# Kernel tuning notes

Hardware: AMD Instinct MI355X
Metric: run time of the kernel (lower is better)

## Reference

```python
import jax, jax.numpy as jnp
import numpy as np

EPS = 1e-6
SEARCH_RANGE = 4  # K = 2*R+1 = 9


def setup_inputs() -> dict:
    key = jax.random.key(0)
    k1, k2, k3, k4 = jax.random.split(key, 4)
    B, C, H, W = 4, 128, 128, 240
    E = 64
    F_L = jax.random.normal(k1, (B, C, H, W), dtype=jnp.float32)
    F_R = jax.random.normal(k2, (B, C, H, W), dtype=jnp.float32)
    d0 = jax.random.uniform(k3, (B, 1, H, W), dtype=jnp.float32) * 64.0  # pixel disparity
    phi_w = jax.random.normal(k4, (E, C), dtype=jnp.float32) / np.sqrt(C)  # 1x1 conv weight
    return {"F_L": F_L, "F_R": F_R, "d0": d0, "phi_w": phi_w}


def _embed(x, phi_w):
    # 1x1 conv + channel L2 normalize (cosine embedding)
    y = jnp.einsum('ec,bchw->behw', phi_w, x)
    norm = jnp.sqrt(jnp.sum(y * y, axis=1, keepdims=True)) + EPS
    return y / norm


def reference(F_L, F_R, d0, phi_w):
    R = SEARCH_RANGE
    FL = _embed(F_L, phi_w)  # (B,E,H,W)
    FR = _embed(F_R, phi_w)
    B, E, H, W = FL.shape
    deltas = jnp.arange(-R, R + 1, dtype=FL.dtype)  # (K,)
    xx = jnp.arange(W, dtype=FL.dtype)  # base x grid
    # x' = x - (d0 + delta); align_corners=True grid round-trips to pixel coords exactly,
    # y coordinate is identity, so warp is 1D bilinear along W with border clamp.
    xprime = xx[None, None, None, :] - d0[:, None, 0, :, :] - deltas[None, :, None, None]  # (B,K,H,W)
    x0 = jnp.floor(xprime)
    w = xprime - x0  # bilinear weight
    i0 = jnp.clip(x0.astype(jnp.int32), 0, W - 1)
    i1 = jnp.clip(x0.astype(jnp.int32) + 1, 0, W - 1)
    FR_e = FR[:, None]  # (B,1,E,H,W)
    g0 = jnp.take_along_axis(FR_e, i0[:, :, None, :, :], axis=4)  # (B,K,E,H,W)
    g1 = jnp.take_along_axis(FR_e, i1[:, :, None, :, :], axis=4)
    FR_s = g0 * (1.0 - w)[:, :, None] + g1 * w[:, :, None]
    cost_vol = jnp.einsum('behw,bkehw->bkhw', FL, FR_s)  # (B,K,H,W)
    return cost_vol
```

## Files before the change

### kernel.cpp

```cpp
#include <hip/hip_runtime.h>

#define NB 4
#define NC 128
#define NH 128
#define NW 240
#define NE 64
#define NK 9
#define PLANE (NH*NW)
#define CHW (NC*PLANE)
#define XS 244

typedef __attribute__((ext_vector_type(8))) short short8;
typedef __attribute__((ext_vector_type(4))) float f32x4;

__device__ __forceinline__ unsigned short f2bf(float f){
  unsigned u = __float_as_uint(f);
  u += 0x7fffu + ((u>>16)&1u);
  return (unsigned short)(u>>16);
}
__device__ __forceinline__ float bfl(unsigned v){ return __uint_as_float(v<<16); }
__device__ __forceinline__ float bfh(unsigned v){ return __uint_as_float(v & 0xffff0000u); }

__global__ __launch_bounds__(256, 1)
void corr_kernel(const float* __restrict__ xL,
                 const float* __restrict__ xR,
                 const float* __restrict__ d0g,
                 const float* __restrict__ phig,
                 float* __restrict__ outg)
{
  __shared__ __attribute__((aligned(16))) unsigned short xs[NC*XS];
  __shared__ __attribute__((aligned(16))) unsigned short phis[NE*136];
  __shared__ __attribute__((aligned(16))) unsigned short FLb[NW*64];
  __shared__ __attribute__((aligned(16))) unsigned short FRb[NW*64];

  const int tid  = threadIdx.x;
  const int lane = tid & 63;
  const int wv   = tid >> 6;
  const int b    = blockIdx.x >> 7;
  const int h    = blockIdx.x & 127;
  const size_t base = (size_t)b*CHW + (size_t)h*NW;

  float d0v = 0.f;
  if (tid < NW) d0v = d0g[(b*NH + h)*NW + tid];

  #pragma unroll
  for (int i = 0; i < 8; ++i) {
    int idx = i*256 + tid;
    int e = idx >> 5, q = idx & 31;
    float4 v = *(const float4*)(phig + e*128 + 4*q);
    uint2 pk;
    pk.x = (unsigned)f2bf(v.x) | ((unsigned)f2bf(v.y) << 16);
    pk.y = (unsigned)f2bf(v.z) | ((unsigned)f2bf(v.w) << 16);
    *(uint2*)&phis[e*136 + 4*q] = pk;
  }

  #pragma unroll
  for (int i = 0; i < 30; ++i) {
    int idx = i*256 + tid;
    int c = idx / 60, s = idx - 60*c;
    float4 v = *(const float4*)(xL + base + (size_t)c*PLANE + 4*s);
    uint2 pk;
    pk.x = (unsigned)f2bf(v.x) | ((unsigned)f2bf(v.y) << 16);
    pk.y = (unsigned)f2bf(v.z) | ((unsigned)f2bf(v.w) << 16);
    *(uint2*)&xs[c*XS + 4*s] = pk;
  }
  __syncthreads();

  const int mrow = lane & 15;
  const int kg   = lane >> 4;
  const int nt0  = wv*4;

  auto gemm_norm = [&](unsigned short* dst) {
    f32x4 acc[4][4];
    #pragma unroll
    for (int i = 0; i < 4; ++i)
      #pragma unroll
      for (int mt = 0; mt < 4; ++mt)
        acc[i][mt] = (f32x4){0.f,0.f,0.f,0.f};

    #pragma unroll
    for (int ks = 0; ks < 4; ++ks) {
      short8 af[4];
      #pragma unroll
      for (int mt = 0; mt < 4; ++mt)
        af[mt] = *(const short8*)&phis[(16*mt + mrow)*136 + 32*ks + 8*kg];
      const int r0 = 32*ks + 8*kg;
      #pragma unroll
      for (int i = 0; i < 4; ++i) {
        int nt = nt0 + i;
        if (nt < 15) {
          int col = 16*nt + mrow;
          short8 bfv;
          #pragma unroll
          for (int j = 0; j < 8; ++j)
            bfv[j] = (short)xs[(r0 + j)*XS + col];
          #pragma unroll
          for (int mt = 0; mt < 4; ++mt)
            acc[i][mt] = __builtin_amdgcn_mfma_f32_16x16x32_bf16(af[mt], bfv, acc[i][mt], 0, 0, 0);
        }
      }
    }
    #pragma unroll
    for (int i = 0; i < 4; ++i) {
      int nt = nt0 + i;
      if (nt >= 15) continue;
      float ss = 0.f;
      #pragma unroll
      for (int mt = 0; mt < 4; ++mt)
        #pragma unroll
        for (int r = 0; r < 4; ++r)
          ss += acc[i][mt][r]*acc[i][mt][r];
      ss += __shfl_xor(ss, 16, 64);
      ss += __shfl_xor(ss, 32, 64);
      float inv = 1.f/(sqrtf(ss) + 1e-6f);
      int n = 16*nt + mrow;
      #pragma unroll
      for (int mt = 0; mt < 4; ++mt) {
        int e0 = 16*mt + 4*kg;
        ushort4 pk;
        pk.x = f2bf(acc[i][mt][0]*inv);
        pk.y = f2bf(acc[i][mt][1]*inv);
        pk.z = f2bf(acc[i][mt][2]*inv);
        pk.w = f2bf(acc[i][mt][3]*inv);
        int pos = n*64 + (((e0>>3) ^ (n&7))<<3) + (e0&7);
        *(ushort4*)&dst[pos] = pk;
      }
    }
  };

  gemm_norm(FLb);
  __syncthreads();

  #pragma unroll
  for (int i = 0; i < 30; ++i) {
    int idx = i*256 + tid;
    int c = idx / 60, s = idx - 60*c;
    float4 v = *(const float4*)(xR + base + (size_t)c*PLANE + 4*s);
    uint2 pk;
    pk.x = (unsigned)f2bf(v.x) | ((unsigned)f2bf(v.y) << 16);
    pk.y = (unsigned)f2bf(v.z) | ((unsigned)f2bf(v.w) << 16);
    *(uint2*)&xs[c*XS + 4*s] = pk;
  }
  __syncthreads();

  gemm_norm(FRb);
  __syncthreads();

  if (tid < NW) {
    const int p = tid;
    float xf  = (float)p - d0v;
    float x0  = floorf(xf);
    float wfr = xf - x0;
    int jb = (int)x0 - 4;

    float fl[64];
    #pragma unroll
    for (int c = 0; c < 8; ++c) {
      uint4 raw = *(const uint4*)&FLb[p*64 + ((c ^ (p&7))<<3)];
      fl[8*c+0]=bfl(raw.x); fl[8*c+1]=bfh(raw.x);
      fl[8*c+2]=bfl(raw.y); fl[8*c+3]=bfh(raw.y);
      fl[8*c+4]=bfl(raw.z); fl[8*c+5]=bfh(raw.z);
      fl[8*c+6]=bfl(raw.w); fl[8*c+7]=bfh(raw.w);
    }

    float D[10];
    #pragma unroll
    for (int t = 0; t < 10; ++t) {
      int j = jb + t;
      j = j < 0 ? 0 : (j > NW-1 ? NW-1 : j);
      float s = 0.f;
      #pragma unroll
      for (int c = 0; c < 8; ++c) {
        uint4 raw = *(const uint4*)&FRb[j*64 + ((c ^ (j&7))<<3)];
        s += fl[8*c+0]*bfl(raw.x) + fl[8*c+1]*bfh(raw.x)
           + fl[8*c+2]*bfl(raw.y) + fl[8*c+3]*bfh(raw.y)
           + fl[8*c+4]*bfl(raw.z) + fl[8*c+5]*bfh(raw.z)
           + fl[8*c+6]*bfl(raw.w) + fl[8*c+7]*bfh(raw.w);
      }
      D[t] = s;
    }

    size_t ob = (size_t)(b*NK)*PLANE + (size_t)h*NW + p;
    #pragma unroll
    for (int k = 0; k < NK; ++k) {
      int t0 = 8 - k;
      float cv = (1.f - wfr)*D[t0] + wfr*D[t0+1];
      outg[ob + (size_t)k*PLANE] = cv;
    }
  }
}

extern "C" void kernel_launch(void* const* d_in, const int* in_sizes, int n_in,
                              void* d_out, int out_size, void* d_ws, size_t ws_size,
                              hipStream_t stream) {
  const float* xL   = (const float*)d_in[0];
  const float* xR   = (const float*)d_in[1];
  const float* d0g  = (const float*)d_in[2];
  const float* phig = (const float*)d_in[3];
  float* outg = (float*)d_out;
  corr_kernel<<<dim3(NB*NH), dim3(256), 0, stream>>>(xL, xR, d0g, phig, outg);
}
```

Measured before the change: 160.4 us.

## Quadruple block size to 1024 threads, one MFMA column tile per wave

Raises the workgroup from 256 to 1024 threads and gives each of the 16 waves one 16-column tile of the embedding GEMM, where before each of 4 waves handled four. Global-to-LDS loads switch to a 64-wide index with a guard instead of a divide by 60. The float-to-bf16 packing now uses the hip_bf16 paired conversion. The aim is more waves per block to hide global load latency and MFMA latency. The catch is that only 15 of 16 waves do GEMM work, and in the final correlation stage just 240 of 1024 threads are active.

```diff
diff --git a/kernel.cpp b/kernel.cpp
--- a/kernel.cpp
+++ b/kernel.cpp
@@ -1,4 +1,5 @@
 #include <hip/hip_runtime.h>
+#include <hip/hip_bf16.h>
 
 #define NB 4
 #define NC 128
@@ -13,6 +14,10 @@
 typedef __attribute__((ext_vector_type(8))) short short8;
 typedef __attribute__((ext_vector_type(4))) float f32x4;
 
+__device__ __forceinline__ unsigned pk2bf(float x, float y){
+  __hip_bfloat162 h = __float22bfloat162_rn(make_float2(x, y));
+  return *(unsigned*)&h;
+}
 __device__ __forceinline__ unsigned short f2bf(float f){
   unsigned u = __float_as_uint(f);
   u += 0x7fffu + ((u>>16)&1u);
@@ -21,7 +26,7 @@
 __device__ __forceinline__ float bfl(unsigned v){ return __uint_as_float(v<<16); }
 __device__ __forceinline__ float bfh(unsigned v){ return __uint_as_float(v & 0xffff0000u); }
 
-__global__ __launch_bounds__(256, 1)
+__global__ __launch_bounds__(1024, 4)
 void corr_kernel(const float* __restrict__ xL,
                  const float* __restrict__ xR,
                  const float* __restrict__ d0g,
@@ -44,72 +49,56 @@
   if (tid < NW) d0v = d0g[(b*NH + h)*NW + tid];
 
   #pragma unroll
-  for (int i = 0; i < 8; ++i) {
-    int idx = i*256 + tid;
+  for (int i = 0; i < 2; ++i) {
+    int idx = i*1024 + tid;
     int e = idx >> 5, q = idx & 31;
     float4 v = *(const float4*)(phig + e*128 + 4*q);
-    uint2 pk;
-    pk.x = (unsigned)f2bf(v.x) | ((unsigned)f2bf(v.y) << 16);
-    pk.y = (unsigned)f2bf(v.z) | ((unsigned)f2bf(v.w) << 16);
+    uint2 pk; pk.x = pk2bf(v.x, v.y); pk.y = pk2bf(v.z, v.w);
     *(uint2*)&phis[e*136 + 4*q] = pk;
   }
 
   #pragma unroll
-  for (int i = 0; i < 30; ++i) {
-    int idx = i*256 + tid;
-    int c = idx / 60, s = idx - 60*c;
-    float4 v = *(const float4*)(xL + base + (size_t)c*PLANE + 4*s);
-    uint2 pk;
-    pk.x = (unsigned)f2bf(v.x) | ((unsigned)f2bf(v.y) << 16);
-    pk.y = (unsigned)f2bf(v.z) | ((unsigned)f2bf(v.w) << 16);
-    *(uint2*)&xs[c*XS + 4*s] = pk;
+  for (int i = 0; i < 8; ++i) {
+    int tau = i*1024 + tid;
+    int c = tau >> 6, s = tau & 63;
+    if (s < 60) {
+      float4 v = *(const float4*)(xL + base + (size_t)c*PLANE + 4*s);
+      uint2 pk; pk.x = pk2bf(v.x, v.y); pk.y = pk2bf(v.z, v.w);
+      *(uint2*)&xs[c*XS + 4*s] = pk;
+    }
   }
   __syncthreads();
 
   const int mrow = lane & 15;
   const int kg   = lane >> 4;
-  const int nt0  = wv*4;
+  const int nt   = wv;
 
   auto gemm_norm = [&](unsigned short* dst) {
-    f32x4 acc[4][4];
+    f32x4 acc[4];
     #pragma unroll
-    for (int i = 0; i < 4; ++i)
+    for (int mt = 0; mt < 4; ++mt) acc[mt] = (f32x4){0.f,0.f,0.f,0.f};
+
+    if (nt < 15) {
+      const int col = 16*nt + mrow;
       #pragma unroll
-      for (int mt = 0; mt < 4; ++mt)
-        acc[i][mt] = (f32x4){0.f,0.f,0.f,0.f};
-
-    #pragma unroll
-    for (int ks = 0; ks < 4; ++ks) {
-      short8 af[4];
-      #pragma unroll
-      for (int mt = 0; mt < 4; ++mt)
-        af[mt] = *(const short8*)&phis[(16*mt + mrow)*136 + 32*ks + 8*kg];
-      const int r0 = 32*ks + 8*kg;
-      #pragma unroll
-      for (int i = 0; i < 4; ++i) {
-        int nt = nt0 + i;
-        if (nt < 15) {
-          int col = 16*nt + mrow;
-          short8 bfv;
-          #pragma unroll
-          for (int j = 0; j < 8; ++j)
-            bfv[j] = (short)xs[(r0 + j)*XS + col];
-          #pragma unroll
-          for (int mt = 0; mt < 4; ++mt)
-            acc[i][mt] = __builtin_amdgcn_mfma_f32_16x16x32_bf16(af[mt], bfv, acc[i][mt], 0, 0, 0);
+      for (int ks = 0; ks < 4; ++ks) {
+        const int r0 = 32*ks + 8*kg;
+        short8 bfv;
+        #pragma unroll
+        for (int j = 0; j < 8; ++j)
+          bfv[j] = (short)xs[(r0 + j)*XS + col];
+        #pragma unroll
+        for (int mt = 0; mt < 4; ++mt) {
+          short8 af = *(const short8*)&phis[(16*mt + mrow)*136 + 32*ks + 8*kg];
+          acc[mt] = __builtin_amdgcn_mfma_f32_16x16x32_bf16(af, bfv, acc[mt], 0, 0, 0);
         }
       }
-    }
-    #pragma unroll
-    for (int i = 0; i < 4; ++i) {
-      int nt = nt0 + i;
-      if (nt >= 15) continue;
       float ss = 0.f;
       #pragma unroll
       for (int mt = 0; mt < 4; ++mt)
         #pragma unroll
         for (int r = 0; r < 4; ++r)
-          ss += acc[i][mt][r]*acc[i][mt][r];
+          ss += acc[mt][r]*acc[mt][r];
       ss += __shfl_xor(ss, 16, 64);
       ss += __shfl_xor(ss, 32, 64);
       float inv = 1.f/(sqrtf(ss) + 1e-6f);
@@ -118,10 +107,10 @@
       for (int mt = 0; mt < 4; ++mt) {
         int e0 = 16*mt + 4*kg;
         ushort4 pk;
-        pk.x = f2bf(acc[i][mt][0]*inv);
-        pk.y = f2bf(acc[i][mt][1]*inv);
-        pk.z = f2bf(acc[i][mt][2]*inv);
-        pk.w = f2bf(acc[i][mt][3]*inv);
+        pk.x = f2bf(acc[mt][0]*inv);
+        pk.y = f2bf(acc[mt][1]*inv);
+        pk.z = f2bf(acc[mt][2]*inv);
+        pk.w = f2bf(acc[mt][3]*inv);
         int pos = n*64 + (((e0>>3) ^ (n&7))<<3) + (e0&7);
         *(ushort4*)&dst[pos] = pk;
       }
@@ -132,14 +121,14 @@
   __syncthreads();
 
   #pragma unroll
-  for (int i = 0; i < 30; ++i) {
-    int idx = i*256 + tid;
-    int c = idx / 60, s = idx - 60*c;
-    float4 v = *(const float4*)(xR + base + (size_t)c*PLANE + 4*s);
-    uint2 pk;
-    pk.x = (unsigned)f2bf(v.x) | ((unsigned)f2bf(v.y) << 16);
-    pk.y = (unsigned)f2bf(v.z) | ((unsigned)f2bf(v.w) << 16);
-    *(uint2*)&xs[c*XS + 4*s] = pk;
+  for (int i = 0; i < 8; ++i) {
+    int tau = i*1024 + tid;
+    int c = tau >> 6, s = tau & 63;
+    if (s < 60) {
+      float4 v = *(const float4*)(xR + base + (size_t)c*PLANE + 4*s);
+      uint2 pk; pk.x = pk2bf(v.x, v.y); pk.y = pk2bf(v.z, v.w);
+      *(uint2*)&xs[c*XS + 4*s] = pk;
+    }
   }
   __syncthreads();
 
@@ -198,5 +187,5 @@
   const float* d0g  = (const float*)d_in[2];
   const float* phig = (const float*)d_in[3];
   float* outg = (float*)d_out;
-  corr_kernel<<<dim3(NB*NH), dim3(256), 0, stream>>>(xL, xR, d0g, phig, outg);
+  corr_kernel<<<dim3(NB*NH), dim3(1024), 0, stream>>>(xL, xR, d0g, phig, outg);
 }
```

After: 158.0 us. No clear change (-1.5%).
